# Optimization experiments

Measured on AMD Instinct MI355X. Metric: run time of the kernel, lower is better.

## Reference

```python
import jax, jax.numpy as jnp
import numpy as np

D_MODEL = 256
D_INNER = 512   # expand=2
D_STATE = 16
DT_RANK = 16    # ceil(d_model/16)
D_CONV = 4
N_LAYERS = 2    # per direction
B, N = 2, 1024


def _mamba_layer(x, W_in, cw, cb, W_x, W_dt, b_dt, A_log, Dp, W_out):
    """One mamba_ssm.Mamba forward. x: (B, L, d_model)."""
    Bb, L, _ = x.shape
    xz = x @ W_in.T                        # (B, L, 2*d_inner)
    di = xz.shape[-1] // 2
    xc, z = xz[..., :di], xz[..., di:]
    # causal depthwise conv1d, kernel D_CONV, left-pad d_conv-1
    K = cw.shape[-1]
    xp = jnp.pad(xc, ((0, 0), (K - 1, 0), (0, 0)))
    xc = sum(xp[:, k:k + L, :] * cw[:, k] for k in range(K)) + cb
    xc = jax.nn.silu(xc)
    # input-dependent dt, B, C
    dbl = xc @ W_x.T                       # (B, L, dt_rank + 2*d_state)
    ds = A_log.shape[-1]
    dt = dbl[..., :DT_RANK]
    Bm = dbl[..., DT_RANK:DT_RANK + ds]    # (B, L, d_state)
    Cm = dbl[..., DT_RANK + ds:]           # (B, L, d_state)
    dt = jax.nn.softplus(dt @ W_dt.T + b_dt)  # (B, L, d_inner)
    A = -jnp.exp(A_log)                    # (d_inner, d_state)
    dA = jnp.exp(dt[..., None] * A)                          # (B, L, di, ds)
    dBx = dt[..., None] * Bm[:, :, None, :] * xc[..., None]  # (B, L, di, ds)

    def step(h, inp):
        a_t, b_t, c_t = inp                # (B,di,ds),(B,di,ds),(B,ds)
        h = a_t * h + b_t
        y_t = jnp.einsum('bds,bs->bd', h, c_t)
        return h, y_t

    h0 = jnp.zeros((Bb, di, ds), x.dtype)
    _, ys = jax.lax.scan(step, h0, (dA.transpose(1, 0, 2, 3),
                                    dBx.transpose(1, 0, 2, 3),
                                    Cm.transpose(1, 0, 2)))
    y = ys.transpose(1, 0, 2) + xc * Dp    # skip term D*x
    y = y * jax.nn.silu(z)                 # gate
    return y @ W_out.T                     # (B, L, d_model)


def setup_inputs() -> dict:
    key = jax.random.key(0)
    ks = jax.random.split(key, 10)
    s = 0.05  # weight scale for numerical stability
    nlay = 2 * N_LAYERS  # forward layers then backward layers
    return {
        "x": jax.random.normal(ks[0], (B, N, D_MODEL), jnp.float32),
        "in_proj": jax.random.normal(ks[1], (nlay, 2 * D_INNER, D_MODEL), jnp.float32) * s,
        "conv_w": jax.random.normal(ks[2], (nlay, D_INNER, D_CONV), jnp.float32) * s,
        "conv_b": jax.random.normal(ks[3], (nlay, D_INNER), jnp.float32) * s,
        "x_proj": jax.random.normal(ks[4], (nlay, DT_RANK + 2 * D_STATE, D_INNER), jnp.float32) * s,
        "dt_proj": jax.random.normal(ks[5], (nlay, D_INNER, DT_RANK), jnp.float32) * s,
        "dt_bias": jax.random.normal(ks[6], (nlay, D_INNER), jnp.float32) * s,
        "A_log": jax.random.uniform(ks[7], (nlay, D_INNER, D_STATE), jnp.float32),
        "D": jax.random.uniform(ks[8], (nlay, D_INNER), jnp.float32),
        "out_proj": jax.random.normal(ks[9], (nlay, D_MODEL, D_INNER), jnp.float32) * s,
    }


def reference(x, in_proj, conv_w, conv_b, x_proj, dt_proj, dt_bias, A_log, D, out_proj):
    n = in_proj.shape[0] // 2
    x_fwd = x
    for i in range(n):
        x_fwd = _mamba_layer(x_fwd, in_proj[i], conv_w[i], conv_b[i], x_proj[i],
                             dt_proj[i], dt_bias[i], A_log[i], D[i], out_proj[i])
    x_bwd = x[:, ::-1, :]
    for i in range(n, 2 * n):
        x_bwd = _mamba_layer(x_bwd, in_proj[i], conv_w[i], conv_b[i], x_proj[i],
                             dt_proj[i], dt_bias[i], A_log[i], D[i], out_proj[i])
    x_bwd = x_bwd[:, ::-1, :]
    return jnp.concatenate([x_fwd, x_bwd], axis=-1)  # (B, N, 2*d_model)
```

## Files before the change

kernel.cpp:

```cpp
#include <hip/hip_runtime.h>
#include <math.h>

#define G 2
#define BB 2
#define L 1024
#define DM 256
#define DI 512
#define DS 16
#define DR 16
#define CH 64
#define CL 16
#define RTOT (G*BB*L)
#define YSTR 520
#define XSTR 520

#define NWIN  (4 * 2 * DI * DM)
#define NWOUT (4 * DM * DI)
#define NWX   (4 * 48 * DI)

typedef short bh8 __attribute__((ext_vector_type(8)));
typedef float f4x __attribute__((ext_vector_type(4)));

#define MFMA16 __builtin_amdgcn_mfma_f32_16x16x32_bf16

__device__ __forceinline__ float silu_f(float x) { return x / (1.f + __expf(-x)); }
__device__ __forceinline__ float softplus_f(float x) {
    return (x > 20.f) ? x : __logf(1.f + __expf(x));
}

__device__ __forceinline__ unsigned short f2bf(float f) {
    unsigned u = __float_as_uint(f);
    unsigned r = u + 0x7FFFu + ((u >> 16) & 1u);
    return (unsigned short)(r >> 16);
}
__device__ __forceinline__ float bf2f(unsigned short s) {
    return __uint_as_float(((unsigned)s) << 16);
}
__device__ __forceinline__ void split4s(float4 v, short4& h, short4& l) {
    unsigned short s;
    s = f2bf(v.x); h.x = (short)s; l.x = (short)f2bf(v.x - bf2f(s));
    s = f2bf(v.y); h.y = (short)s; l.y = (short)f2bf(v.y - bf2f(s));
    s = f2bf(v.z); h.z = (short)s; l.z = (short)f2bf(v.z - bf2f(s));
    s = f2bf(v.w); h.w = (short)s; l.w = (short)f2bf(v.w - bf2f(s));
}

template<int AMAP>
__global__ __launch_bounds__(256) void mfma_inproj(
    const float* __restrict__ Ax,
    const short* __restrict__ APh, const short* __restrict__ APl,
    const float* __restrict__ WinF,
    const short* __restrict__ Wh, const short* __restrict__ Wl,
    int step, float* __restrict__ C,
    const float* __restrict__ cvtA, short* __restrict__ cAh, short* __restrict__ cAl, int n4a,
    const float* __restrict__ cvtB, short* __restrict__ cBh, short* __restrict__ cBl, int n4b,
    const float* __restrict__ cvtC, short* __restrict__ cCh, short* __restrict__ cCl, int n4c)
{
    constexpr int BM = 128, Ktot = DM, Nout = 2 * DI, ldc = 1024;
    __shared__ short As_hi[BM * 40];
    __shared__ short As_lo[BM * 40];
    __shared__ short Bs_hi[64 * 40];
    __shared__ short Bs_lo[64 * 40];

    const int row0 = blockIdx.y * BM;
    const int col0 = blockIdx.x * 64;
    const int g    = row0 >> 11;
    const int lay  = g * 2 + step;
    const short* Whg = Wh  + (size_t)lay * Nout * Ktot;
    const short* Wlg = Wl  + (size_t)lay * Nout * Ktot;
    const float* WFg = WinF + (size_t)lay * Nout * Ktot;
    const int t    = threadIdx.x;
    const int lane = t & 63, wv = t >> 6;
    const int m = lane & 15, quad = lane >> 4;
    const int wr = wv >> 1, wc = wv & 1;
    const int NT = Ktot / 32;

    float4 pa[4];
    short4 pah[4], pal[4], pbh[2], pbl[2];
    float4 pbf[2];
    auto loadT = [&](int kt) {
        const int kb = kt * 32;
        #pragma unroll
        for (int i = 0; i < 4; i++) {
            int id = t + 256 * i;
            int row = id >> 3, kq = id & 7;
            if (AMAP == 1) {
                int gr = row0 + row;
                int gg = gr >> 11, b = (gr >> 10) & 1, l = gr & 1023;
                int sl = gg ? (1023 - l) : l;
                pa[i] = *(const float4*)&Ax[(size_t)(b * 1024 + sl) * Ktot + kb + kq * 4];
            } else {
                size_t o = (size_t)(row0 + row) * Ktot + kb + kq * 4;
                pah[i] = *(const short4*)&APh[o];
                pal[i] = *(const short4*)&APl[o];
            }
        }
        #pragma unroll
        for (int i = 0; i < 2; i++) {
            int id = t + 256 * i;
            int row = id >> 3, kq = id & 7;
            if (AMAP == 1) {
                pbf[i] = *(const float4*)&WFg[(size_t)(col0 + row) * Ktot + kb + kq * 4];
            } else {
                size_t o = (size_t)(col0 + row) * Ktot + kb + kq * 4;
                pbh[i] = *(const short4*)&Whg[o];
                pbl[i] = *(const short4*)&Wlg[o];
            }
        }
    };

    f4x acc[4][2] = {};
    loadT(0);

    for (int kt = 0; kt < NT; kt++) {
        #pragma unroll
        for (int i = 0; i < 4; i++) {
            int id = t + 256 * i;
            int row = id >> 3, kq = id & 7;
            if (AMAP == 1) {
                short4 h4, l4; split4s(pa[i], h4, l4);
                *(short4*)&As_hi[row * 40 + kq * 4] = h4;
                *(short4*)&As_lo[row * 40 + kq * 4] = l4;
            } else {
                *(short4*)&As_hi[row * 40 + kq * 4] = pah[i];
                *(short4*)&As_lo[row * 40 + kq * 4] = pal[i];
            }
        }
        #pragma unroll
        for (int i = 0; i < 2; i++) {
            int id = t + 256 * i;
            int row = id >> 3, kq = id & 7;
            if (AMAP == 1) {
                short4 h4, l4; split4s(pbf[i], h4, l4);
                *(short4*)&Bs_hi[row * 40 + kq * 4] = h4;
                *(short4*)&Bs_lo[row * 40 + kq * 4] = l4;
            } else {
                *(short4*)&Bs_hi[row * 40 + kq * 4] = pbh[i];
                *(short4*)&Bs_lo[row * 40 + kq * 4] = pbl[i];
            }
        }
        __syncthreads();
        if (kt + 1 < NT) loadT(kt + 1);

        bh8 ah[4], al[4], bh[2], bl[2];
        #pragma unroll
        for (int p = 0; p < 4; p++) {
            int r = wr * 64 + p * 16 + m;
            ah[p] = *(bh8*)&As_hi[r * 40 + quad * 8];
            al[p] = *(bh8*)&As_lo[r * 40 + quad * 8];
        }
        #pragma unroll
        for (int q = 0; q < 2; q++) {
            int r = wc * 32 + q * 16 + m;
            bh[q] = *(bh8*)&Bs_hi[r * 40 + quad * 8];
            bl[q] = *(bh8*)&Bs_lo[r * 40 + quad * 8];
        }
        #pragma unroll
        for (int p = 0; p < 4; p++)
            #pragma unroll
            for (int q = 0; q < 2; q++) {
                acc[p][q] = MFMA16(ah[p], bh[q], acc[p][q], 0, 0, 0);
                acc[p][q] = MFMA16(ah[p], bl[q], acc[p][q], 0, 0, 0);
                acc[p][q] = MFMA16(al[p], bh[q], acc[p][q], 0, 0, 0);
            }
        __syncthreads();
    }

    #pragma unroll
    for (int p = 0; p < 4; p++)
        #pragma unroll
        for (int q = 0; q < 2; q++) {
            int gcol = col0 + wc * 32 + q * 16 + m;
            #pragma unroll
            for (int r = 0; r < 4; r++) {
                int grow = row0 + wr * 64 + p * 16 + quad * 4 + r;
                C[(size_t)grow * ldc + gcol] = acc[p][q][r];
            }
        }

    if (AMAP == 1) {
        const int bid = blockIdx.y * 16 + blockIdx.x;
        const int ntot = n4a + n4b + n4c;
        for (int i = bid * 256 + t; i < ntot; i += 512 * 256) {
            int j = i; const float* W; short *H, *Lo;
            if (j < n4a) { W = cvtA; H = cAh; Lo = cAl; }
            else if (j < n4a + n4b) { j -= n4a; W = cvtB; H = cBh; Lo = cBl; }
            else { j -= n4a + n4b; W = cvtC; H = cCh; Lo = cCl; }
            float4 v = *(const float4*)&W[(size_t)j * 4];
            short4 h4, l4; split4s(v, h4, l4);
            *(short4*)&H[(size_t)j * 4] = h4;
            *(short4*)&Lo[(size_t)j * 4] = l4;
        }
    }
}

__global__ __launch_bounds__(512) void scanA2(
    const float* __restrict__ XZ, const float* __restrict__ cw,
    const float* __restrict__ cb,
    const short* __restrict__ Wxh, const short* __restrict__ Wxl,
    const float* __restrict__ A_log, const float* __restrict__ Wdt,
    const float* __restrict__ bdt,
    float* __restrict__ XCb, float* __restrict__ DBLc,
    float* __restrict__ Aprod, float* __restrict__ Hend, int step)
{
    __shared__ short xcH[CL * XSTR];
    __shared__ short xcL[CL * XSTR];
    __shared__ float part[8][CL][48];
    __shared__ float dbl[CL][48];

    const int blk = blockIdx.x;
    const int c  = blk & (CH - 1);
    const int gb = blk >> 6;
    const int g  = gb >> 1;
    const int lay = g * 2 + step;
    const int d  = threadIdx.x;
    const int r0 = gb * L + c * CL;

    float4 w4 = *(const float4*)&cw[((size_t)lay * DI + d) * 4];
    float cbv = cb[(size_t)lay * DI + d];
    float xz[CL + 3];
    #pragma unroll
    for (int j = 0; j < CL + 3; j++) {
        int lr = c * CL + j - 3;
        xz[j] = (lr < 0) ? 0.f : XZ[(size_t)(gb * L + lr) * 1024 + d];
    }
    float xc[CL];
    #pragma unroll
    for (int tt = 0; tt < CL; tt++) {
        float v = cbv + w4.x * xz[tt] + w4.y * xz[tt + 1]
                      + w4.z * xz[tt + 2] + w4.w * xz[tt + 3];
        v = silu_f(v);
        xc[tt] = v;
        XCb[(size_t)(r0 + tt) * DI + d] = v;
        unsigned short hs = f2bf(v);
        xcH[tt * XSTR + d] = (short)hs;
        xcL[tt * XSTR + d] = (short)f2bf(v - bf2f(hs));
    }
    __syncthreads();

    {
        const int lane = d & 63, wv = d >> 6;
        const int m = lane & 15, quad = lane >> 4;
        const int ks = wv * 64;
        const size_t wb = (size_t)lay * 48 * DI;
        f4x acc3[3] = {};
        #pragma unroll
        for (int kt = 0; kt < 2; kt++) {
            const int kb = ks + kt * 32 + quad * 8;
            bh8 ah = *(bh8*)&xcH[m * XSTR + kb];
            bh8 al = *(bh8*)&xcL[m * XSTR + kb];
            #pragma unroll
            for (int f = 0; f < 3; f++) {
                bh8 bh = *(const bh8*)&Wxh[wb + (size_t)(f * 16 + m) * DI + kb];
                bh8 bl = *(const bh8*)&Wxl[wb + (size_t)(f * 16 + m) * DI + kb];
                acc3[f] = MFMA16(ah, bh, acc3[f], 0, 0, 0);
                acc3[f] = MFMA16(ah, bl, acc3[f], 0, 0, 0);
                acc3[f] = MFMA16(al, bh, acc3[f], 0, 0, 0);
            }
        }
        #pragma unroll
        for (int f = 0; f < 3; f++)
            #pragma unroll
            for (int r = 0; r < 4; r++)
                part[wv][quad * 4 + r][f * 16 + m] = acc3[f][r];
    }
    __syncthreads();

    for (int o = d; o < CL * 48; o += 512) {
        int tt = o / 48, cc = o - tt * 48;
        float v = 0.f;
        #pragma unroll
        for (int w = 0; w < 8; w++) v += part[w][tt][cc];
        dbl[tt][cc] = v;
        DBLc[(size_t)(r0 + tt) * 48 + cc] = v;
    }

    float wdt[16];
    const float* wrow = Wdt + ((size_t)lay * DI + d) * DR;
    #pragma unroll
    for (int k = 0; k < 16; k += 4) {
        float4 v = *(const float4*)&wrow[k];
        wdt[k] = v.x; wdt[k + 1] = v.y; wdt[k + 2] = v.z; wdt[k + 3] = v.w;
    }
    float bias = bdt[(size_t)lay * DI + d];

    float a[DS], h[DS], ap[DS];
    const float* al = A_log + ((size_t)lay * DI + d) * DS;
    #pragma unroll
    for (int s = 0; s < DS; s++) { a[s] = -__expf(al[s]); h[s] = 0.f; ap[s] = 1.f; }
    __syncthreads();

    for (int tt = 0; tt < CL; tt++) {
        float dtr = bias;
        #pragma unroll
        for (int k = 0; k < 16; k++) dtr += dbl[tt][k] * wdt[k];
        float dt = softplus_f(dtr);
        float dx = dt * xc[tt];
        #pragma unroll
        for (int s = 0; s < DS; s++) {
            float da = __expf(dt * a[s]);
            h[s] = da * h[s] + dx * dbl[tt][16 + s];
            ap[s] *= da;
        }
    }
    size_t base = ((size_t)(gb * DI + d) * CH + c) * DS;
    #pragma unroll
    for (int q = 0; q < 4; q++) {
        *(float4*)&Aprod[base + q * 4] = make_float4(ap[q*4], ap[q*4+1], ap[q*4+2], ap[q*4+3]);
        *(float4*)&Hend [base + q * 4] = make_float4(h[q*4],  h[q*4+1],  h[q*4+2],  h[q*4+3]);
    }
}

__global__ __launch_bounds__(256) void scanCombine(
    const float* __restrict__ Aprod, const float* __restrict__ Hend,
    float* __restrict__ Hinit)
{
    int idx = blockIdx.x * 256 + threadIdx.x;
    int s  = idx & 15;
    int gd = idx >> 4;
    size_t base = (size_t)gd * CH * DS + s;
    float h = 0.f;
    for (int c0 = 0; c0 < CH; c0 += 8) {
        float ap[8], e[8];
        #pragma unroll
        for (int j = 0; j < 8; j++) {
            size_t o = base + (size_t)(c0 + j) * DS;
            ap[j] = Aprod[o]; e[j] = Hend[o];
        }
        #pragma unroll
        for (int j = 0; j < 8; j++) {
            Hinit[base + (size_t)(c0 + j) * DS] = h;
            h = ap[j] * h + e[j];
        }
    }
}

template<int OUTMODE>
__global__ __launch_bounds__(512) void scanB_fused(
    const float* __restrict__ XCb, const float* __restrict__ DBLc,
    const float* __restrict__ XZ, const float* __restrict__ A_log,
    const float* __restrict__ Wdt, const float* __restrict__ bdt,
    const float* __restrict__ Dp, const float* __restrict__ Hinit,
    const short* __restrict__ Woh, const short* __restrict__ Wol,
    float* __restrict__ Cout, short* __restrict__ Ph, short* __restrict__ Pl,
    int step)
{
    __shared__ float dbl[CL][48];
    __shared__ short Ys_hi[CL * YSTR];
    __shared__ short Ys_lo[CL * YSTR];
    int blk = blockIdx.x;
    int c  = blk & (CH - 1);
    int gb = blk >> 6;
    int g  = gb >> 1;
    int lay = g * 2 + step;
    int d = threadIdx.x;
    int r0 = gb * L + c * CL;

    for (int id = threadIdx.x; id < CL * 48; id += 512) {
        int rr = id / 48, cc = id - rr * 48;
        dbl[rr][cc] = DBLc[(size_t)(r0 + rr) * 48 + cc];
    }

    float xc[CL], zz[CL];
    #pragma unroll
    for (int tt = 0; tt < CL; tt++) xc[tt] = XCb[(size_t)(r0 + tt) * DI + d];
    #pragma unroll
    for (int tt = 0; tt < CL; tt++) zz[tt] = XZ[(size_t)(r0 + tt) * 1024 + 512 + d];

    float wdt[16];
    const float* wrow = Wdt + ((size_t)lay * DI + d) * DR;
    #pragma unroll
    for (int k = 0; k < 16; k += 4) {
        float4 v = *(const float4*)&wrow[k];
        wdt[k] = v.x; wdt[k + 1] = v.y; wdt[k + 2] = v.z; wdt[k + 3] = v.w;
    }
    float bias = bdt[(size_t)lay * DI + d];

    float a[DS], h[DS];
    const float* al = A_log + ((size_t)lay * DI + d) * DS;
    size_t base = ((size_t)(gb * DI + d) * CH + c) * DS;
    #pragma unroll
    for (int q = 0; q < 4; q++) {
        float4 hv = *(const float4*)&Hinit[base + q * 4];
        h[q*4] = hv.x; h[q*4+1] = hv.y; h[q*4+2] = hv.z; h[q*4+3] = hv.w;
    }
    #pragma unroll
    for (int s = 0; s < DS; s++) a[s] = -__expf(al[s]);
    float Dv = Dp[(size_t)lay * DI + d];
    __syncthreads();

    #pragma unroll
    for (int tt = 0; tt < CL; tt++) {
        float dtr = bias;
        #pragma unroll
        for (int k = 0; k < 16; k++) dtr += dbl[tt][k] * wdt[k];
        float dt = softplus_f(dtr);
        float dx = dt * xc[tt];
        float y = 0.f;
        #pragma unroll
        for (int s = 0; s < DS; s++) {
            float da = __expf(dt * a[s]);
            h[s] = da * h[s] + dx * dbl[tt][16 + s];
            y += h[s] * dbl[tt][32 + s];
        }
        y += xc[tt] * Dv;
        y *= silu_f(zz[tt]);
        unsigned short hs = f2bf(y);
        Ys_hi[tt * YSTR + d] = (short)hs;
        Ys_lo[tt * YSTR + d] = (short)f2bf(y - bf2f(hs));
    }
    __syncthreads();

    const int lane = threadIdx.x & 63, wv = threadIdx.x >> 6;
    const int m = lane & 15, quad = lane >> 4;
    const size_t wbase = (size_t)lay * DM * DI;

    #pragma unroll
    for (int q = 0; q < 2; q++) {
        const int coln = wv * 32 + q * 16 + m;
        const size_t wrow2 = wbase + (size_t)coln * DI;
        bh8 wh[16], wl[16];
        #pragma unroll
        for (int i = 0; i < 16; i++) {
            const int kk = i * 32 + quad * 8;
            wh[i] = *(const bh8*)&Woh[wrow2 + kk];
            wl[i] = *(const bh8*)&Wol[wrow2 + kk];
        }
        f4x acc = {};
        #pragma unroll
        for (int i = 0; i < 16; i++) {
            const int kk = i * 32 + quad * 8;
            bh8 ahv = *(bh8*)&Ys_hi[m * YSTR + kk];
            bh8 alv = *(bh8*)&Ys_lo[m * YSTR + kk];
            acc = MFMA16(ahv, wh[i], acc, 0, 0, 0);
            acc = MFMA16(ahv, wl[i], acc, 0, 0, 0);
            acc = MFMA16(alv, wh[i], acc, 0, 0, 0);
        }
        #pragma unroll
        for (int r = 0; r < 4; r++) {
            int tt = quad * 4 + r;
            int grow = r0 + tt;
            if (OUTMODE == 0) {
                size_t o = (size_t)grow * DM + coln;
                unsigned short hs = f2bf(acc[r]);
                Ph[o] = (short)hs;
                Pl[o] = (short)f2bf(acc[r] - bf2f(hs));
            } else {
                int b = (grow >> 10) & 1, l = grow & 1023;
                size_t dst = (g == 0)
                    ? ((size_t)(b * 1024 + l) * 512 + coln)
                    : ((size_t)(b * 1024 + (1023 - l)) * 512 + 256 + coln);
                Cout[dst] = acc[r];
            }
        }
    }
}

extern "C" void kernel_launch(void* const* d_in, const int* in_sizes, int n_in,
                              void* d_out, int out_size, void* d_ws, size_t ws_size,
                              hipStream_t stream)
{
    const float* x        = (const float*)d_in[0];
    const float* in_proj  = (const float*)d_in[1];
    const float* conv_w   = (const float*)d_in[2];
    const float* conv_b   = (const float*)d_in[3];
    const float* x_proj   = (const float*)d_in[4];
    const float* dt_proj  = (const float*)d_in[5];
    const float* dt_bias  = (const float*)d_in[6];
    const float* A_log    = (const float*)d_in[7];
    const float* Dp       = (const float*)d_in[8];
    const float* out_proj = (const float*)d_in[9];
    float* out = (float*)d_out;

    float* w = (float*)d_ws;
    size_t o = 0;
    float* XZ    = w + o; o += (size_t)RTOT * 1024;
    float* XCb   = w + o; o += (size_t)RTOT * DI;
    float* DBLc  = w + o; o += (size_t)RTOT * 48;
    float* Aprod = w + o; o += (size_t)G * BB * DI * CH * DS;
    float* Hend  = w + o; o += (size_t)G * BB * DI * CH * DS;
    float* Hinit = w + o; o += (size_t)G * BB * DI * CH * DS;
    short* Wih   = (short*)(w + o); o += NWIN / 2;
    short* Wil   = (short*)(w + o); o += NWIN / 2;
    short* Woh   = (short*)(w + o); o += NWOUT / 2;
    short* Wol   = (short*)(w + o); o += NWOUT / 2;
    short* Wxh   = (short*)(w + o); o += NWX / 2;
    short* Wxl   = (short*)(w + o); o += NWX / 2;
    short* Ph    = (short*)(w + o); o += (size_t)RTOT * DM / 2;
    short* Pl    = (short*)(w + o); o += (size_t)RTOT * DM / 2;
    (void)ws_size; (void)in_sizes; (void)n_in; (void)out_size;

    for (int step = 0; step < 2; step++) {
        if (step == 0)
            mfma_inproj<1><<<dim3(16, 32), 256, 0, stream>>>(
                x, nullptr, nullptr, in_proj, nullptr, nullptr, 0, XZ,
                in_proj, Wih, Wil, NWIN / 4,
                out_proj, Woh, Wol, NWOUT / 4,
                x_proj, Wxh, Wxl, NWX / 4);
        else
            mfma_inproj<0><<<dim3(16, 32), 256, 0, stream>>>(
                nullptr, Ph, Pl, nullptr, Wih, Wil, 1, XZ,
                nullptr, nullptr, nullptr, 0,
                nullptr, nullptr, nullptr, 0,
                nullptr, nullptr, nullptr, 0);

        scanA2<<<G * BB * CH, 512, 0, stream>>>(
            XZ, conv_w, conv_b, Wxh, Wxl, A_log, dt_proj, dt_bias,
            XCb, DBLc, Aprod, Hend, step);

        scanCombine<<<(G * BB * DI * DS) / 256, 256, 0, stream>>>(Aprod, Hend, Hinit);

        if (step == 0)
            scanB_fused<0><<<G * BB * CH, 512, 0, stream>>>(
                XCb, DBLc, XZ, A_log, dt_proj, dt_bias, Dp, Hinit,
                Woh, Wol, nullptr, Ph, Pl, 0);
        else
            scanB_fused<1><<<G * BB * CH, 512, 0, stream>>>(
                XCb, DBLc, XZ, A_log, dt_proj, dt_bias, Dp, Hinit,
                Woh, Wol, out, nullptr, nullptr, 1);
    }
}
```

Before: 222.5 us.

## Fuse chunk scan, combine, and output pass into one cooperative kernel

Merges scanA2, scanCombine and scanB_fused into a single cooperatively launched kernel. Blocks synchronise through per-batch atomic counters and spin-waits, so the intermediate xc, dbl and dt values stay in registers and shared memory instead of being written to global and read back. The scan combine is spread across blocks, each handling 8 channels. This removes two kernel launches and the XCb/DBLc global round-trips, at the cost of grid-wide spin barriers that depend on all 256 blocks being resident, plus more shared memory per block through a union buffer.

New measurement: 711.4 us. +219.7%, slower.

```diff
diff --git a/kernel.cpp b/kernel.cpp
--- a/kernel.cpp
+++ b/kernel.cpp
@@ -53,7 +53,8 @@
     int step, float* __restrict__ C,
     const float* __restrict__ cvtA, short* __restrict__ cAh, short* __restrict__ cAl, int n4a,
     const float* __restrict__ cvtB, short* __restrict__ cBh, short* __restrict__ cBl, int n4b,
-    const float* __restrict__ cvtC, short* __restrict__ cCh, short* __restrict__ cCl, int n4c)
+    const float* __restrict__ cvtC, short* __restrict__ cCh, short* __restrict__ cCl, int n4c,
+    unsigned* __restrict__ Ctr)
 {
     constexpr int BM = 128, Ktot = DM, Nout = 2 * DI, ldc = 1024;
     __shared__ short As_hi[BM * 40];
@@ -179,6 +180,7 @@
 
     if (AMAP == 1) {
         const int bid = blockIdx.y * 16 + blockIdx.x;
+        if (bid == 0 && t < 16) Ctr[t] = 0u;
         const int ntot = n4a + n4b + n4c;
         for (int i = bid * 256 + t; i < ntot; i += 512 * 256) {
             int j = i; const float* W; short *H, *Lo;
@@ -193,19 +195,27 @@
     }
 }
 
-__global__ __launch_bounds__(512) void scanA2(
+template<int OUTMODE>
+__global__ __launch_bounds__(512) void scanAB(
     const float* __restrict__ XZ, const float* __restrict__ cw,
     const float* __restrict__ cb,
     const short* __restrict__ Wxh, const short* __restrict__ Wxl,
     const float* __restrict__ A_log, const float* __restrict__ Wdt,
-    const float* __restrict__ bdt,
-    float* __restrict__ XCb, float* __restrict__ DBLc,
-    float* __restrict__ Aprod, float* __restrict__ Hend, int step)
+    const float* __restrict__ bdt, const float* __restrict__ Dp,
+    float* __restrict__ Aprod, float* __restrict__ Hend,
+    float* __restrict__ Hinit,
+    unsigned* __restrict__ ctrA, unsigned* __restrict__ ctrB,
+    const short* __restrict__ Woh, const short* __restrict__ Wol,
+    float* __restrict__ Cout, short* __restrict__ Ph, short* __restrict__ Pl,
+    int step)
 {
-    __shared__ short xcH[CL * XSTR];
-    __shared__ short xcL[CL * XSTR];
-    __shared__ float part[8][CL][48];
     __shared__ float dbl[CL][48];
+    __shared__ __align__(16) char uni[57856];
+    short* xcH  = (short*)uni;
+    short* xcL  = xcH + CL * XSTR;
+    float* part = (float*)(uni + 33280);
+    short* Ys_hi = (short*)uni;
+    short* Ys_lo = Ys_hi + CL * YSTR;
 
     const int blk = blockIdx.x;
     const int c  = blk & (CH - 1);
@@ -213,24 +223,26 @@
     const int g  = gb >> 1;
     const int lay = g * 2 + step;
     const int d  = threadIdx.x;
+    const int tid = threadIdx.x;
     const int r0 = gb * L + c * CL;
+    const int lane = tid & 63, wv = tid >> 6;
+    const int m = lane & 15, quad = lane >> 4;
 
     float4 w4 = *(const float4*)&cw[((size_t)lay * DI + d) * 4];
     float cbv = cb[(size_t)lay * DI + d];
-    float xz[CL + 3];
+    float xzv[CL + 3];
     #pragma unroll
     for (int j = 0; j < CL + 3; j++) {
         int lr = c * CL + j - 3;
-        xz[j] = (lr < 0) ? 0.f : XZ[(size_t)(gb * L + lr) * 1024 + d];
+        xzv[j] = (lr < 0) ? 0.f : XZ[(size_t)(gb * L + lr) * 1024 + d];
     }
     float xc[CL];
     #pragma unroll
     for (int tt = 0; tt < CL; tt++) {
-        float v = cbv + w4.x * xz[tt] + w4.y * xz[tt + 1]
-                      + w4.z * xz[tt + 2] + w4.w * xz[tt + 3];
+        float v = cbv + w4.x * xzv[tt] + w4.y * xzv[tt + 1]
+                      + w4.z * xzv[tt + 2] + w4.w * xzv[tt + 3];
         v = silu_f(v);
         xc[tt] = v;
-        XCb[(size_t)(r0 + tt) * DI + d] = v;
         unsigned short hs = f2bf(v);
         xcH[tt * XSTR + d] = (short)hs;
         xcL[tt * XSTR + d] = (short)f2bf(v - bf2f(hs));
@@ -238,8 +250,6 @@
     __syncthreads();
 
     {
-        const int lane = d & 63, wv = d >> 6;
-        const int m = lane & 15, quad = lane >> 4;
         const int ks = wv * 64;
         const size_t wb = (size_t)lay * 48 * DI;
         f4x acc3[3] = {};
@@ -261,17 +271,16 @@
         for (int f = 0; f < 3; f++)
             #pragma unroll
             for (int r = 0; r < 4; r++)
-                part[wv][quad * 4 + r][f * 16 + m] = acc3[f][r];
-    }
-    __syncthreads();
-
-    for (int o = d; o < CL * 48; o += 512) {
+                part[(wv * CL + quad * 4 + r) * 48 + f * 16 + m] = acc3[f][r];
+    }
+    __syncthreads();
+
+    for (int o = tid; o < CL * 48; o += 512) {
         int tt = o / 48, cc = o - tt * 48;
         float v = 0.f;
         #pragma unroll
-        for (int w = 0; w < 8; w++) v += part[w][tt][cc];
+        for (int w = 0; w < 8; w++) v += part[(w * CL + tt) * 48 + cc];
         dbl[tt][cc] = v;
-        DBLc[(size_t)(r0 + tt) * 48 + cc] = v;
     }
 
     float wdt[16];
@@ -283,7 +292,7 @@
     }
     float bias = bdt[(size_t)lay * DI + d];
 
-    float a[DS], h[DS], ap[DS];
+    float a[DS], h[DS], ap[DS], dts[CL];
     const float* al = A_log + ((size_t)lay * DI + d) * DS;
     #pragma unroll
     for (int s = 0; s < DS; s++) { a[s] = -__expf(al[s]); h[s] = 0.f; ap[s] = 1.f; }
@@ -294,6 +303,7 @@
         #pragma unroll
         for (int k = 0; k < 16; k++) dtr += dbl[tt][k] * wdt[k];
         float dt = softplus_f(dtr);
+        dts[tt] = dt;
         float dx = dt * xc[tt];
         #pragma unroll
         for (int s = 0; s < DS; s++) {
@@ -308,92 +318,65 @@
         *(float4*)&Aprod[base + q * 4] = make_float4(ap[q*4], ap[q*4+1], ap[q*4+2], ap[q*4+3]);
         *(float4*)&Hend [base + q * 4] = make_float4(h[q*4],  h[q*4+1],  h[q*4+2],  h[q*4+3]);
     }
-}
-
-__global__ __launch_bounds__(256) void scanCombine(
-    const float* __restrict__ Aprod, const float* __restrict__ Hend,
-    float* __restrict__ Hinit)
-{
-    int idx = blockIdx.x * 256 + threadIdx.x;
-    int s  = idx & 15;
-    int gd = idx >> 4;
-    size_t base = (size_t)gd * CH * DS + s;
-    float h = 0.f;
-    for (int c0 = 0; c0 < CH; c0 += 8) {
-        float ap[8], e[8];
-        #pragma unroll
-        for (int j = 0; j < 8; j++) {
-            size_t o = base + (size_t)(c0 + j) * DS;
-            ap[j] = Aprod[o]; e[j] = Hend[o];
-        }
-        #pragma unroll
-        for (int j = 0; j < 8; j++) {
-            Hinit[base + (size_t)(c0 + j) * DS] = h;
-            h = ap[j] * h + e[j];
-        }
-    }
-}
-
-template<int OUTMODE>
-__global__ __launch_bounds__(512) void scanB_fused(
-    const float* __restrict__ XCb, const float* __restrict__ DBLc,
-    const float* __restrict__ XZ, const float* __restrict__ A_log,
-    const float* __restrict__ Wdt, const float* __restrict__ bdt,
-    const float* __restrict__ Dp, const float* __restrict__ Hinit,
-    const short* __restrict__ Woh, const short* __restrict__ Wol,
-    float* __restrict__ Cout, short* __restrict__ Ph, short* __restrict__ Pl,
-    int step)
-{
-    __shared__ float dbl[CL][48];
-    __shared__ short Ys_hi[CL * YSTR];
-    __shared__ short Ys_lo[CL * YSTR];
-    int blk = blockIdx.x;
-    int c  = blk & (CH - 1);
-    int gb = blk >> 6;
-    int g  = gb >> 1;
-    int lay = g * 2 + step;
-    int d = threadIdx.x;
-    int r0 = gb * L + c * CL;
-
-    for (int id = threadIdx.x; id < CL * 48; id += 512) {
-        int rr = id / 48, cc = id - rr * 48;
-        dbl[rr][cc] = DBLc[(size_t)(r0 + rr) * 48 + cc];
-    }
-
-    float xc[CL], zz[CL];
-    #pragma unroll
-    for (int tt = 0; tt < CL; tt++) xc[tt] = XCb[(size_t)(r0 + tt) * DI + d];
+
+    __threadfence();
+    __syncthreads();
+    if (tid == 0) atomicAdd(&ctrA[gb], 1u);
+
+    float zz[CL];
     #pragma unroll
     for (int tt = 0; tt < CL; tt++) zz[tt] = XZ[(size_t)(r0 + tt) * 1024 + 512 + d];
-
-    float wdt[16];
-    const float* wrow = Wdt + ((size_t)lay * DI + d) * DR;
-    #pragma unroll
-    for (int k = 0; k < 16; k += 4) {
-        float4 v = *(const float4*)&wrow[k];
-        wdt[k] = v.x; wdt[k + 1] = v.y; wdt[k + 2] = v.z; wdt[k + 3] = v.w;
-    }
-    float bias = bdt[(size_t)lay * DI + d];
-
-    float a[DS], h[DS];
-    const float* al = A_log + ((size_t)lay * DI + d) * DS;
-    size_t base = ((size_t)(gb * DI + d) * CH + c) * DS;
+    float Dv = Dp[(size_t)lay * DI + d];
+
+    if (tid == 0) {
+        unsigned it = 0;
+        while (__hip_atomic_load(&ctrA[gb], __ATOMIC_RELAXED,
+                                 __HIP_MEMORY_SCOPE_AGENT) < 64u &&
+               ++it < (1u << 26)) __builtin_amdgcn_s_sleep(8);
+    }
+    __syncthreads();
+    __threadfence();
+
+    if (tid < 128) {
+        int dd = c * 8 + (tid >> 4);
+        int ss = tid & 15;
+        size_t b2 = (size_t)(gb * DI + dd) * CH * DS + ss;
+        float hh = 0.f;
+        for (int c0 = 0; c0 < CH; c0 += 8) {
+            float apv[8], ev[8];
+            #pragma unroll
+            for (int j = 0; j < 8; j++) {
+                size_t o = b2 + (size_t)(c0 + j) * DS;
+                apv[j] = Aprod[o]; ev[j] = Hend[o];
+            }
+            #pragma unroll
+            for (int j = 0; j < 8; j++) {
+                Hinit[b2 + (size_t)(c0 + j) * DS] = hh;
+                hh = apv[j] * hh + ev[j];
+            }
+        }
+    }
+    __threadfence();
+    __syncthreads();
+    if (tid == 0) atomicAdd(&ctrB[gb], 1u);
+
+    if (tid == 0) {
+        unsigned it = 0;
+        while (__hip_atomic_load(&ctrB[gb], __ATOMIC_RELAXED,
+                                 __HIP_MEMORY_SCOPE_AGENT) < 64u &&
+               ++it < (1u << 26)) __builtin_amdgcn_s_sleep(8);
+    }
+    __syncthreads();
+    __threadfence();
+
     #pragma unroll
     for (int q = 0; q < 4; q++) {
         float4 hv = *(const float4*)&Hinit[base + q * 4];
         h[q*4] = hv.x; h[q*4+1] = hv.y; h[q*4+2] = hv.z; h[q*4+3] = hv.w;
     }
     #pragma unroll
-    for (int s = 0; s < DS; s++) a[s] = -__expf(al[s]);
-    float Dv = Dp[(size_t)lay * DI + d];
-    __syncthreads();
-
-    #pragma unroll
     for (int tt = 0; tt < CL; tt++) {
-        float dtr = bias;
-        #pragma unroll
-        for (int k = 0; k < 16; k++) dtr += dbl[tt][k] * wdt[k];
-        float dt = softplus_f(dtr);
+        float dt = dts[tt];
         float dx = dt * xc[tt];
         float y = 0.f;
         #pragma unroll
@@ -410,10 +393,7 @@
     }
     __syncthreads();
 
-    const int lane = threadIdx.x & 63, wv = threadIdx.x >> 6;
-    const int m = lane & 15, quad = lane >> 4;
     const size_t wbase = (size_t)lay * DM * DI;
-
     #pragma unroll
     for (int q = 0; q < 2; q++) {
         const int coln = wv * 32 + q * 16 + m;
@@ -474,8 +454,6 @@
     float* w = (float*)d_ws;
     size_t o = 0;
     float* XZ    = w + o; o += (size_t)RTOT * 1024;
-    float* XCb   = w + o; o += (size_t)RTOT * DI;
-    float* DBLc  = w + o; o += (size_t)RTOT * 48;
     float* Aprod = w + o; o += (size_t)G * BB * DI * CH * DS;
     float* Hend  = w + o; o += (size_t)G * BB * DI * CH * DS;
     float* Hinit = w + o; o += (size_t)G * BB * DI * CH * DS;
@@ -487,6 +465,8 @@
     short* Wxl   = (short*)(w + o); o += NWX / 2;
     short* Ph    = (short*)(w + o); o += (size_t)RTOT * DM / 2;
     short* Pl    = (short*)(w + o); o += (size_t)RTOT * DM / 2;
+    o = (o + 63) & ~(size_t)63;
+    unsigned* Ctr = (unsigned*)(w + o); o += 64;
     (void)ws_size; (void)in_sizes; (void)n_in; (void)out_size;
 
     for (int step = 0; step < 2; step++) {
@@ -495,27 +475,46 @@
                 x, nullptr, nullptr, in_proj, nullptr, nullptr, 0, XZ,
                 in_proj, Wih, Wil, NWIN / 4,
                 out_proj, Woh, Wol, NWOUT / 4,
-                x_proj, Wxh, Wxl, NWX / 4);
+                x_proj, Wxh, Wxl, NWX / 4, Ctr);
         else
             mfma_inproj<0><<<dim3(16, 32), 256, 0, stream>>>(
                 nullptr, Ph, Pl, nullptr, Wih, Wil, 1, XZ,
                 nullptr, nullptr, nullptr, 0,
                 nullptr, nullptr, nullptr, 0,
-                nullptr, nullptr, nullptr, 0);
-
-        scanA2<<<G * BB * CH, 512, 0, stream>>>(
-            XZ, conv_w, conv_b, Wxh, Wxl, A_log, dt_proj, dt_bias,
-            XCb, DBLc, Aprod, Hend, step);
-
-        scanCombine<<<(G * BB * DI * DS) / 256, 256, 0, stream>>>(Aprod, Hend, Hinit);
-
-        if (step == 0)
-            scanB_fused<0><<<G * BB * CH, 512, 0, stream>>>(
-                XCb, DBLc, XZ, A_log, dt_proj, dt_bias, Dp, Hinit,
-                Woh, Wol, nullptr, Ph, Pl, 0);
-        else
-            scanB_fused<1><<<G * BB * CH, 512, 0, stream>>>(
-                XCb, DBLc, XZ, A_log, dt_proj, dt_bias, Dp, Hinit,
-                Woh, Wol, out, nullptr, nullptr, 1);
-    }
-}
+                nullptr, nullptr, nullptr, 0, nullptr);
+
+        unsigned* ctrA = Ctr + step * 8;
+        unsigned* ctrB = ctrA + 4;
+        const float* XZc = XZ;
+        const short *Wxhc = Wxh, *Wxlc = Wxl, *Wohc = Woh, *Wolc = Wol;
+        float* Coutp = (step == 0) ? nullptr : out;
+        short* Php = (step == 0) ? Ph : nullptr;
+        short* Plp = (step == 0) ? Pl : nullptr;
+        int stepv = step;
+        void* kargs[] = {
+            (void*)&XZc, (void*)&conv_w, (void*)&conv_b,
+            (void*)&Wxhc, (void*)&Wxlc, (void*)&A_log, (void*)&dt_proj,
+            (void*)&dt_bias, (void*)&Dp,
+            (void*)&Aprod, (void*)&Hend, (void*)&Hinit,
+            (void*)&ctrA, (void*)&ctrB,
+            (void*)&Wohc, (void*)&Wolc,
+            (void*)&Coutp, (void*)&Php, (void*)&Plp, (void*)&stepv };
+        void* fn = (step == 0) ? reinterpret_cast<void*>(scanAB<0>)
+                               : reinterpret_cast<void*>(scanAB<1>);
+        hipError_t err = hipLaunchCooperativeKernel(
+            fn, dim3(G * BB * CH), dim3(512), kargs, 0, stream);
+        if (err != hipSuccess) {
+            (void)hipGetLastError();
+            if (step == 0)
+                scanAB<0><<<G * BB * CH, 512, 0, stream>>>(
+                    XZ, conv_w, conv_b, Wxh, Wxl, A_log, dt_proj, dt_bias, Dp,
+                    Aprod, Hend, Hinit, ctrA, ctrB, Woh, Wol,
+                    nullptr, Ph, Pl, 0);
+            else
+                scanAB<1><<<G * BB * CH, 512, 0, stream>>>(
+                    XZ, conv_w, conv_b, Wxh, Wxl, A_log, dt_proj, dt_bias, Dp,
+                    Aprod, Hend, Hinit, ctrA, ctrB, Woh, Wol,
+                    out, nullptr, nullptr, 1);
+        }
+    }
+}
```
